# Kernel optimization log

Measured on AMD Instinct MI355X. Metric: run time of the kernel, lower is better.

## Reference

```python
import jax, jax.numpy as jnp
import numpy as np

B, L, H = 64, 1024, 512  # batch, seq_len, hidden_units; encoder feature = 2H


def setup_inputs() -> dict:
    key = jax.random.key(0)
    k1, k2, k3, k4, k5 = jax.random.split(key, 5)
    scale = 1.0 / np.sqrt(3 * H)
    return {
        "hidden": jax.random.normal(k1, (B, H), dtype=jnp.float32),
        "encoder_outputs": jax.random.normal(k2, (B, L, 2 * H), dtype=jnp.float32),
        "W_attn": jax.random.normal(k3, (3 * H, H), dtype=jnp.float32) * scale,
        "b_attn": jax.random.normal(k4, (H,), dtype=jnp.float32) * scale,
        "W_v": jax.random.normal(k5, (H, 1), dtype=jnp.float32) * (1.0 / np.sqrt(H)),
    }


def reference(hidden, encoder_outputs, W_attn, b_attn, W_v):
    # hidden: [B, H] broadcast along seq -> [B, L, H] (torch repeat+transpose)
    b, l, e = encoder_outputs.shape
    h_rep = jnp.broadcast_to(hidden[:, None, :], (b, l, hidden.shape[-1]))
    cat = jnp.concatenate([h_rep, encoder_outputs], axis=-1)     # [B, L, 3H]
    energy = jax.nn.relu(cat @ W_attn + b_attn)                  # [B, L, H]
    attention = (energy @ W_v)[..., 0]                           # [B, L]
    weights = jax.nn.softmax(attention, axis=1)                  # [B, L]
    # bmm([B,1,L], [B,L,E]) -> [B,1,E]
    context = jnp.einsum("bl,ble->be", weights, encoder_outputs)[:, None, :]
    return context
```

## Files before the change

### kernel.cpp

```cpp
#include <hip/hip_runtime.h>
#include <hip/hip_bf16.h>

typedef __attribute__((ext_vector_type(8))) __bf16 bf16x8;
typedef __attribute__((ext_vector_type(4))) float f32x4;


__global__ void qk(const float* __restrict__ hidden, const float* __restrict__ W_attn,
                   const float* __restrict__ b_attn, float* __restrict__ q) {
    int idx = blockIdx.x * 256 + threadIdx.x;
    int b = idx >> 9;
    int h = idx & 511;
    const float* hv = hidden + b * 512;
    float acc = b_attn[h];
#pragma unroll 8
    for (int k = 0; k < 512; ++k)
        acc = fmaf(hv[k], W_attn[(size_t)k * 512 + h], acc);
    q[idx] = acc;
}

__global__ void btk(const float* __restrict__ W_attn, __bf16* __restrict__ Bt) {
    int idx = blockIdx.x * 256 + threadIdx.x;
    int n = idx >> 10;
    int k = idx & 1023;
    Bt[idx] = (__bf16)W_attn[(size_t)(512 + k) * 512 + n];
}

__global__ __launch_bounds__(256, 2) void gemm_logits(
    const float* __restrict__ A, const __bf16* __restrict__ Bt,
    const float* __restrict__ q, const float* __restrict__ Wv,
    float* __restrict__ part)
{
    __shared__ __bf16 As[128][64];
    __shared__ __bf16 Bs[128][64];
    __shared__ float red[128][2];

    const int bid = blockIdx.x;
    const int swz = (bid & 7) * 256 + (bid >> 3);
    const int mt = swz >> 2;
    const int nt = swz & 3;

    const int t = threadIdx.x;
    const int lane = t & 63;
    const int wid = t >> 6;
    const int wm = wid >> 1;
    const int wn = wid & 1;

    const int ar = t >> 3;
    const int ac = (t & 7) * 8;
    const float* Ag = A + (size_t)(mt * 128 + ar) * 1024 + ac;
    const __bf16* Bg = Bt + (size_t)(nt * 128 + ar) * 1024 + ac;

    f32x4 acc[4][4];
#pragma unroll
    for (int m = 0; m < 4; ++m)
#pragma unroll
        for (int n = 0; n < 4; ++n) acc[m][n] = (f32x4)0.0f;

    float4 a0[4], a1[4];
    bf16x8 bv[4];

#define LOADS(K0)                                                              \
    {                                                                          \
        _Pragma("unroll") for (int i = 0; i < 4; ++i) {                        \
            const float* p = Ag + (size_t)i * 32768 + (K0);                    \
            a0[i] = *(const float4*)p;                                         \
            a1[i] = *(const float4*)(p + 4);                                   \
            bv[i] = *(const bf16x8*)(Bg + (size_t)i * 32768 + (K0));           \
        }                                                                      \
    }

    LOADS(0)

    for (int k0 = 0; k0 < 1024; k0 += 64) {
        __syncthreads();
#pragma unroll
        for (int i = 0; i < 4; ++i) {
            bf16x8 v;
            v[0] = (__bf16)a0[i].x; v[1] = (__bf16)a0[i].y;
            v[2] = (__bf16)a0[i].z; v[3] = (__bf16)a0[i].w;
            v[4] = (__bf16)a1[i].x; v[5] = (__bf16)a1[i].y;
            v[6] = (__bf16)a1[i].z; v[7] = (__bf16)a1[i].w;
            *(bf16x8*)&As[ar + i * 32][ac] = v;
            *(bf16x8*)&Bs[ar + i * 32][ac] = bv[i];
        }
        __syncthreads();

        int kn = k0 + 64;
        if (kn < 1024) LOADS(kn)

        const int rsel = (lane & 15);
        const int kb = (lane >> 4) * 8;
#pragma unroll
        for (int ks = 0; ks < 2; ++ks) {
            bf16x8 af[4], bg[4];
#pragma unroll
            for (int m = 0; m < 4; ++m)
                af[m] = *(const bf16x8*)&As[wm * 64 + m * 16 + rsel][ks * 32 + kb];
#pragma unroll
            for (int n = 0; n < 4; ++n)
                bg[n] = *(const bf16x8*)&Bs[wn * 64 + n * 16 + rsel][ks * 32 + kb];
#pragma unroll
            for (int m = 0; m < 4; ++m)
#pragma unroll
                for (int n = 0; n < 4; ++n)
                    acc[m][n] = __builtin_amdgcn_mfma_f32_16x16x32_bf16(
                        af[m], bg[n], acc[m][n], 0, 0, 0);
        }
    }
#undef LOADS

    const int b = mt >> 3;
    const float* qb = q + b * 512;
    float qv[4], wvv[4];
#pragma unroll
    for (int n = 0; n < 4; ++n) {
        int gc = nt * 128 + wn * 64 + n * 16 + (lane & 15);
        qv[n] = qb[gc];
        wvv[n] = Wv[gc];
    }

#pragma unroll
    for (int m = 0; m < 4; ++m) {
#pragma unroll
        for (int j = 0; j < 4; ++j) {
            float s = 0.f;
#pragma unroll
            for (int n = 0; n < 4; ++n) {
                float e = acc[m][n][j] + qv[n];
                s += (e > 0.f ? e : 0.f) * wvv[n];
            }
            s += __shfl_xor(s, 1);
            s += __shfl_xor(s, 2);
            s += __shfl_xor(s, 4);
            s += __shfl_xor(s, 8);
            if ((lane & 15) == 0) {
                int r = wm * 64 + m * 16 + (lane >> 4) * 4 + j;
                red[r][wn] = s;
            }
        }
    }
    __syncthreads();
    if (t < 128) {
        float v = red[t][0] + red[t][1];
        part[(size_t)nt * 65536 + (size_t)mt * 128 + t] = v;
    }
}

__global__ void softmax_k(const float* __restrict__ part, float* __restrict__ w) {
    __shared__ float smx[4];
    __shared__ float ssum[4];
    int b = blockIdx.x;
    int t = threadIdx.x;
    int lane = t & 63, wid = t >> 6;
    float v[4];
    float mx = -3.0e38f;
#pragma unroll
    for (int i = 0; i < 4; ++i) {
        int l = t + i * 256;
        int o = b * 1024 + l;
        float s = part[o] + part[65536 + o] + part[131072 + o] + part[196608 + o];
        v[i] = s;
        mx = fmaxf(mx, s);
    }
#pragma unroll
    for (int off = 32; off >= 1; off >>= 1) mx = fmaxf(mx, __shfl_xor(mx, off));
    if (lane == 0) smx[wid] = mx;
    __syncthreads();
    mx = fmaxf(fmaxf(smx[0], smx[1]), fmaxf(smx[2], smx[3]));
    float e[4];
    float sum = 0.f;
#pragma unroll
    for (int i = 0; i < 4; ++i) { e[i] = __expf(v[i] - mx); sum += e[i]; }
#pragma unroll
    for (int off = 32; off >= 1; off >>= 1) sum += __shfl_xor(sum, off);
    if (lane == 0) ssum[wid] = sum;
    __syncthreads();
    float inv = 1.f / (ssum[0] + ssum[1] + ssum[2] + ssum[3]);
#pragma unroll
    for (int i = 0; i < 4; ++i) w[b * 1024 + t + i * 256] = e[i] * inv;
}

__global__ void ctx_partial(const float* __restrict__ enc, const float* __restrict__ w,
                            float* __restrict__ ctxp) {
    int blk = blockIdx.x;
    int b = blk >> 3;
    int lc = blk & 7;
    int t = threadIdx.x;
    __shared__ float wl[128];
    if (t < 128) wl[t] = w[b * 1024 + lc * 128 + t];
    __syncthreads();
    float4 acc = {0.f, 0.f, 0.f, 0.f};
    const float* base = enc + ((size_t)(b * 1024 + lc * 128)) * 1024 + t * 4;
    for (int l = 0; l < 128; ++l) {
        float4 v = *(const float4*)(base + (size_t)l * 1024);
        float s = wl[l];
        acc.x += s * v.x; acc.y += s * v.y; acc.z += s * v.z; acc.w += s * v.w;
    }
    *(float4*)(ctxp + (size_t)(lc * 64 + b) * 1024 + t * 4) = acc;
}

__global__ void ctx_sum(const float* __restrict__ ctxp, float* __restrict__ out) {
    int idx = blockIdx.x * 256 + threadIdx.x;
    float4 a = {0.f, 0.f, 0.f, 0.f};
#pragma unroll
    for (int lc = 0; lc < 8; ++lc) {
        float4 v = *(const float4*)(ctxp + (size_t)lc * 65536 + (size_t)idx * 4);
        a.x += v.x; a.y += v.y; a.z += v.z; a.w += v.w;
    }
    *(float4*)(out + (size_t)idx * 4) = a;
}

extern "C" void kernel_launch(void* const* d_in, const int* in_sizes, int n_in,
                              void* d_out, int out_size, void* d_ws, size_t ws_size,
                              hipStream_t stream) {
    const float* hidden = (const float*)d_in[0];
    const float* enc    = (const float*)d_in[1];
    const float* W_attn = (const float*)d_in[2];
    const float* b_attn = (const float*)d_in[3];
    const float* W_v    = (const float*)d_in[4];
    float* out = (float*)d_out;

    char* ws = (char*)d_ws;
    float*  q    = (float*)(ws + 0);
    __bf16* Bt   = (__bf16*)(ws + 131072);
    float*  part = (float*)(ws + 1179648);
    float*  wts  = (float*)(ws + 2228224);
    float*  ctxp = (float*)(ws + 2490368);

    qk<<<128, 256, 0, stream>>>(hidden, W_attn, b_attn, q);
    btk<<<2048, 256, 0, stream>>>(W_attn, Bt);
    gemm_logits<<<2048, 256, 0, stream>>>(enc, Bt, q, W_v, part);
    softmax_k<<<64, 256, 0, stream>>>(part, wts);
    ctx_partial<<<512, 256, 0, stream>>>(enc, wts, ctxp);
    ctx_sum<<<64, 256, 0, stream>>>(ctxp, out);
}
```

Before: 192.5 us.

## Compute full N per block with LDS-direct B loads and double buffering

The logits GEMM now gives each 512-thread block the full 512-wide N dimension for a 128-row M tile. Before, four N tiles each re-read and re-converted the same fp32 encoder rows, so those redundant reads are gone, along with the partial-logit buffer and its summation in softmax. The weight matrix is pre-laid out as padded K-tiles (KPAD 40) and streamed into LDS with global_load_lds, double-buffered across 32 K-steps of 32, with one barrier per step. The cost is a much larger LDS footprint and accumulator register set, and only 512 blocks, which may limit occupancy and latency hiding.

```diff
diff --git a/kernel.cpp b/kernel.cpp
--- a/kernel.cpp
+++ b/kernel.cpp
@@ -4,6 +4,9 @@
 typedef __attribute__((ext_vector_type(8))) __bf16 bf16x8;
 typedef __attribute__((ext_vector_type(4))) float f32x4;
 
+
+#define KPAD 40
+#define NKT 32
 
 __global__ void qk(const float* __restrict__ hidden, const float* __restrict__ W_attn,
                    const float* __restrict__ b_attn, float* __restrict__ q) {
@@ -18,103 +21,113 @@
     q[idx] = acc;
 }
 
-__global__ void btk(const float* __restrict__ W_attn, __bf16* __restrict__ Bt) {
+__global__ void btk_img(const float* __restrict__ W_attn, __bf16* __restrict__ Bimg) {
     int idx = blockIdx.x * 256 + threadIdx.x;
-    int n = idx >> 10;
-    int k = idx & 1023;
-    Bt[idx] = (__bf16)W_attn[(size_t)(512 + k) * 512 + n];
-}
-
-__global__ __launch_bounds__(256, 2) void gemm_logits(
-    const float* __restrict__ A, const __bf16* __restrict__ Bt,
-    const float* __restrict__ q, const float* __restrict__ Wv,
-    float* __restrict__ part)
+    int kt = idx / (512 * KPAD);
+    int r  = idx % (512 * KPAD);
+    int n  = r / KPAD;
+    int kk = r % KPAD;
+    float v = (kk < 32) ? W_attn[(size_t)(512 + kt * 32 + kk) * 512 + n] : 0.f;
+    Bimg[idx] = (__bf16)v;
+}
+
+__device__ inline void gl_lds16(const void* g, void* l) {
+    __builtin_amdgcn_global_load_lds(
+        (const __attribute__((address_space(1))) void*)g,
+        (__attribute__((address_space(3))) void*)l, 16, 0, 0);
+}
+
+__global__ __launch_bounds__(512, 2) void gemm_logits2(
+    const float* __restrict__ A,
+    const __bf16* __restrict__ Bimg,
+    const float* __restrict__ q,
+    const float* __restrict__ Wv,
+    float* __restrict__ logits)
 {
-    __shared__ __bf16 As[128][64];
-    __shared__ __bf16 Bs[128][64];
-    __shared__ float red[128][2];
+    __shared__ __bf16 As[2][128 * KPAD];
+    __shared__ __bf16 Bs[2][512 * KPAD];
+    __shared__ float red[128][4];
 
     const int bid = blockIdx.x;
-    const int swz = (bid & 7) * 256 + (bid >> 3);
-    const int mt = swz >> 2;
-    const int nt = swz & 3;
-
+    const int mt = (bid & 7) * 64 + (bid >> 3);
     const int t = threadIdx.x;
     const int lane = t & 63;
     const int wid = t >> 6;
-    const int wm = wid >> 1;
-    const int wn = wid & 1;
-
-    const int ar = t >> 3;
-    const int ac = (t & 7) * 8;
-    const float* Ag = A + (size_t)(mt * 128 + ar) * 1024 + ac;
-    const __bf16* Bg = Bt + (size_t)(nt * 128 + ar) * 1024 + ac;
-
-    f32x4 acc[4][4];
+    const int wm = wid >> 2;
+    const int wn = wid & 3;
+
+    const int ar = t >> 2;
+    const int ak = (t & 3) * 8;
+    const float* Ag = A + (size_t)(mt * 128 + ar) * 1024 + ak;
+    __bf16* AwrBase0 = &As[0][ar * KPAD + ak];
+    __bf16* AwrBase1 = &As[1][ar * KPAD + ak];
+
+    const __bf16* Bg = Bimg + (size_t)(wid * 5) * 512 + lane * 8;
+
+    f32x4 acc[4][8];
 #pragma unroll
     for (int m = 0; m < 4; ++m)
 #pragma unroll
-        for (int n = 0; n < 4; ++n) acc[m][n] = (f32x4)0.0f;
-
-    float4 a0[4], a1[4];
-    bf16x8 bv[4];
-
-#define LOADS(K0)                                                              \
+        for (int n = 0; n < 8; ++n) acc[m][n] = (f32x4)0.0f;
+
+    const int rsel = lane & 15;
+    const int kb = (lane >> 4) * 8;
+
+#define STAGE_B(KT, BUF)                                                       \
     {                                                                          \
-        _Pragma("unroll") for (int i = 0; i < 4; ++i) {                        \
-            const float* p = Ag + (size_t)i * 32768 + (K0);                    \
-            a0[i] = *(const float4*)p;                                         \
-            a1[i] = *(const float4*)(p + 4);                                   \
-            bv[i] = *(const bf16x8*)(Bg + (size_t)i * 32768 + (K0));           \
-        }                                                                      \
-    }
-
-    LOADS(0)
-
-    for (int k0 = 0; k0 < 1024; k0 += 64) {
-        __syncthreads();
-#pragma unroll
-        for (int i = 0; i < 4; ++i) {
+        const __bf16* src = Bg + (size_t)(KT) * (512 * KPAD);                  \
+        _Pragma("unroll") for (int i = 0; i < 5; ++i)                          \
+            gl_lds16(src + i * 512, &Bs[BUF][(wid * 5 + i) * 512]);            \
+    }
+
+    STAGE_B(0, 0)
+    float4 p0 = *(const float4*)Ag;
+    float4 p1 = *(const float4*)(Ag + 4);
+    {
+        bf16x8 v;
+        v[0] = (__bf16)p0.x; v[1] = (__bf16)p0.y; v[2] = (__bf16)p0.z; v[3] = (__bf16)p0.w;
+        v[4] = (__bf16)p1.x; v[5] = (__bf16)p1.y; v[6] = (__bf16)p1.z; v[7] = (__bf16)p1.w;
+        *(bf16x8*)AwrBase0 = v;
+    }
+    __syncthreads();
+
+    for (int kt = 0; kt < NKT; ++kt) {
+        const int cur = kt & 1;
+        if (kt + 1 < NKT) {
+            STAGE_B(kt + 1, cur ^ 1)
+            const float* p = Ag + (kt + 1) * 32;
+            p0 = *(const float4*)p;
+            p1 = *(const float4*)(p + 4);
+        }
+
+        bf16x8 af[4];
+#pragma unroll
+        for (int m = 0; m < 4; ++m)
+            af[m] = *(const bf16x8*)&As[cur][(wm * 64 + m * 16 + rsel) * KPAD + kb];
+#pragma unroll
+        for (int n = 0; n < 8; ++n) {
+            bf16x8 bg = *(const bf16x8*)&Bs[cur][(wn * 128 + n * 16 + rsel) * KPAD + kb];
+#pragma unroll
+            for (int m = 0; m < 4; ++m)
+                acc[m][n] = __builtin_amdgcn_mfma_f32_16x16x32_bf16(
+                    af[m], bg, acc[m][n], 0, 0, 0);
+        }
+
+        if (kt + 1 < NKT) {
             bf16x8 v;
-            v[0] = (__bf16)a0[i].x; v[1] = (__bf16)a0[i].y;
-            v[2] = (__bf16)a0[i].z; v[3] = (__bf16)a0[i].w;
-            v[4] = (__bf16)a1[i].x; v[5] = (__bf16)a1[i].y;
-            v[6] = (__bf16)a1[i].z; v[7] = (__bf16)a1[i].w;
-            *(bf16x8*)&As[ar + i * 32][ac] = v;
-            *(bf16x8*)&Bs[ar + i * 32][ac] = bv[i];
-        }
-        __syncthreads();
-
-        int kn = k0 + 64;
-        if (kn < 1024) LOADS(kn)
-
-        const int rsel = (lane & 15);
-        const int kb = (lane >> 4) * 8;
-#pragma unroll
-        for (int ks = 0; ks < 2; ++ks) {
-            bf16x8 af[4], bg[4];
-#pragma unroll
-            for (int m = 0; m < 4; ++m)
-                af[m] = *(const bf16x8*)&As[wm * 64 + m * 16 + rsel][ks * 32 + kb];
-#pragma unroll
-            for (int n = 0; n < 4; ++n)
-                bg[n] = *(const bf16x8*)&Bs[wn * 64 + n * 16 + rsel][ks * 32 + kb];
-#pragma unroll
-            for (int m = 0; m < 4; ++m)
-#pragma unroll
-                for (int n = 0; n < 4; ++n)
-                    acc[m][n] = __builtin_amdgcn_mfma_f32_16x16x32_bf16(
-                        af[m], bg[n], acc[m][n], 0, 0, 0);
-        }
-    }
-#undef LOADS
-
-    const int b = mt >> 3;
-    const float* qb = q + b * 512;
-    float qv[4], wvv[4];
-#pragma unroll
-    for (int n = 0; n < 4; ++n) {
-        int gc = nt * 128 + wn * 64 + n * 16 + (lane & 15);
+            v[0] = (__bf16)p0.x; v[1] = (__bf16)p0.y; v[2] = (__bf16)p0.z; v[3] = (__bf16)p0.w;
+            v[4] = (__bf16)p1.x; v[5] = (__bf16)p1.y; v[6] = (__bf16)p1.z; v[7] = (__bf16)p1.w;
+            *(bf16x8*)((cur ^ 1) ? AwrBase1 : AwrBase0) = v;
+            __syncthreads();
+        }
+    }
+#undef STAGE_B
+
+    const float* qb = q + (mt >> 3) * 512;
+    float qv[8], wvv[8];
+#pragma unroll
+    for (int n = 0; n < 8; ++n) {
+        int gc = wn * 128 + n * 16 + rsel;
         qv[n] = qb[gc];
         wvv[n] = Wv[gc];
     }
@@ -125,7 +138,7 @@
         for (int j = 0; j < 4; ++j) {
             float s = 0.f;
 #pragma unroll
-            for (int n = 0; n < 4; ++n) {
+            for (int n = 0; n < 8; ++n) {
                 float e = acc[m][n][j] + qv[n];
                 s += (e > 0.f ? e : 0.f) * wvv[n];
             }
@@ -133,20 +146,18 @@
             s += __shfl_xor(s, 2);
             s += __shfl_xor(s, 4);
             s += __shfl_xor(s, 8);
-            if ((lane & 15) == 0) {
+            if (rsel == 0) {
                 int r = wm * 64 + m * 16 + (lane >> 4) * 4 + j;
                 red[r][wn] = s;
             }
         }
     }
     __syncthreads();
-    if (t < 128) {
-        float v = red[t][0] + red[t][1];
-        part[(size_t)nt * 65536 + (size_t)mt * 128 + t] = v;
-    }
-}
-
-__global__ void softmax_k(const float* __restrict__ part, float* __restrict__ w) {
+    if (t < 128)
+        logits[(size_t)mt * 128 + t] = red[t][0] + red[t][1] + red[t][2] + red[t][3];
+}
+
+__global__ void softmax_k(const float* __restrict__ logits, float* __restrict__ w) {
     __shared__ float smx[4];
     __shared__ float ssum[4];
     int b = blockIdx.x;
@@ -156,9 +167,7 @@
     float mx = -3.0e38f;
 #pragma unroll
     for (int i = 0; i < 4; ++i) {
-        int l = t + i * 256;
-        int o = b * 1024 + l;
-        float s = part[o] + part[65536 + o] + part[131072 + o] + part[196608 + o];
+        float s = logits[b * 1024 + t + i * 256];
         v[i] = s;
         mx = fmaxf(mx, s);
     }
@@ -221,16 +230,16 @@
     float* out = (float*)d_out;
 
     char* ws = (char*)d_ws;
-    float*  q    = (float*)(ws + 0);
-    __bf16* Bt   = (__bf16*)(ws + 131072);
-    float*  part = (float*)(ws + 1179648);
-    float*  wts  = (float*)(ws + 2228224);
-    float*  ctxp = (float*)(ws + 2490368);
+    float*  q      = (float*)(ws + 0);
+    __bf16* Bimg   = (__bf16*)(ws + 131072);
+    float*  logits = (float*)(ws + 1441792);
+    float*  wts    = (float*)(ws + 1703936);
+    float*  ctxp   = (float*)(ws + 1966080);
 
     qk<<<128, 256, 0, stream>>>(hidden, W_attn, b_attn, q);
-    btk<<<2048, 256, 0, stream>>>(W_attn, Bt);
-    gemm_logits<<<2048, 256, 0, stream>>>(enc, Bt, q, W_v, part);
-    softmax_k<<<64, 256, 0, stream>>>(part, wts);
+    btk_img<<<2560, 256, 0, stream>>>(W_attn, Bimg);
+    gemm_logits2<<<512, 512, 0, stream>>>(enc, Bimg, q, W_v, logits);
+    softmax_k<<<64, 256, 0, stream>>>(logits, wts);
     ctx_partial<<<512, 256, 0, stream>>>(enc, wts, ctxp);
     ctx_sum<<<64, 256, 0, stream>>>(ctxp, out);
 }
```

Result: slower. 201.8 us (+4.8%).

## Double-buffer GEMM LDS tiles with padded rows and smaller K step

Applied to the files above, without the earlier changes.

Reworks the logits GEMM to use two LDS buffers with a K tile of 32 and padded row stride (40), so each iteration needs only one barrier and the next tile's global loads overlap the MFMA work. Padding is meant to reduce LDS bank conflicts on the fragment reads. Launch bounds are raised to 4 blocks per CU and the reduction scratch reuses the B buffer. The cost is more loop iterations and barriers per K, plus register pressure under the tighter occupancy target.

```diff
diff --git a/kernel.cpp b/kernel.cpp
--- a/kernel.cpp
+++ b/kernel.cpp
@@ -2,8 +2,12 @@
 #include <hip/hip_bf16.h>
 
 typedef __attribute__((ext_vector_type(8))) __bf16 bf16x8;
+typedef __attribute__((ext_vector_type(4))) __bf16 bf16x4;
 typedef __attribute__((ext_vector_type(4))) float f32x4;
 
+
+#define KPAD 40
+#define NKT 32
 
 __global__ void qk(const float* __restrict__ hidden, const float* __restrict__ W_attn,
                    const float* __restrict__ b_attn, float* __restrict__ q) {
@@ -25,14 +29,14 @@
     Bt[idx] = (__bf16)W_attn[(size_t)(512 + k) * 512 + n];
 }
 
-__global__ __launch_bounds__(256, 2) void gemm_logits(
+__global__ __launch_bounds__(256, 4) void gemm_logits3(
     const float* __restrict__ A, const __bf16* __restrict__ Bt,
     const float* __restrict__ q, const float* __restrict__ Wv,
     float* __restrict__ part)
 {
-    __shared__ __bf16 As[128][64];
-    __shared__ __bf16 Bs[128][64];
-    __shared__ float red[128][2];
+    __shared__ __bf16 As[2][128 * KPAD];
+    __shared__ __bf16 Bs[2][128 * KPAD];
+    float* red = (float*)&Bs[0][0];
 
     const int bid = blockIdx.x;
     const int swz = (bid & 7) * 256 + (bid >> 3);
@@ -46,9 +50,11 @@
     const int wn = wid & 1;
 
     const int ar = t >> 3;
-    const int ac = (t & 7) * 8;
+    const int ac = (t & 7) * 4;
     const float* Ag = A + (size_t)(mt * 128 + ar) * 1024 + ac;
-    const __bf16* Bg = Bt + (size_t)(nt * 128 + ar) * 1024 + ac;
+    const int br = t >> 2;
+    const int bc = (t & 3) * 8;
+    const __bf16* Bg = Bt + (size_t)(nt * 128 + br) * 1024 + bc;
 
     f32x4 acc[4][4];
 #pragma unroll
@@ -56,65 +62,69 @@
 #pragma unroll
         for (int n = 0; n < 4; ++n) acc[m][n] = (f32x4)0.0f;
 
-    float4 a0[4], a1[4];
-    bf16x8 bv[4];
+    float4 av[4];
+    bf16x8 bv[2];
 
 #define LOADS(K0)                                                              \
     {                                                                          \
+        _Pragma("unroll") for (int i = 0; i < 4; ++i)                          \
+            av[i] = *(const float4*)(Ag + (size_t)i * 32768 + (K0));           \
+        _Pragma("unroll") for (int i = 0; i < 2; ++i)                          \
+            bv[i] = *(const bf16x8*)(Bg + (size_t)i * 65536 + (K0));           \
+    }
+
+#define WRITES(BUF)                                                            \
+    {                                                                          \
         _Pragma("unroll") for (int i = 0; i < 4; ++i) {                        \
-            const float* p = Ag + (size_t)i * 32768 + (K0);                    \
-            a0[i] = *(const float4*)p;                                         \
-            a1[i] = *(const float4*)(p + 4);                                   \
-            bv[i] = *(const bf16x8*)(Bg + (size_t)i * 32768 + (K0));           \
+            bf16x4 w;                                                          \
+            w[0] = (__bf16)av[i].x; w[1] = (__bf16)av[i].y;                    \
+            w[2] = (__bf16)av[i].z; w[3] = (__bf16)av[i].w;                    \
+            *(bf16x4*)&As[BUF][(ar + i * 32) * KPAD + ac] = w;                 \
         }                                                                      \
+        _Pragma("unroll") for (int i = 0; i < 2; ++i)                          \
+            *(bf16x8*)&Bs[BUF][(br + i * 64) * KPAD + bc] = bv[i];             \
     }
 
     LOADS(0)
-
-    for (int k0 = 0; k0 < 1024; k0 += 64) {
-        __syncthreads();
-#pragma unroll
-        for (int i = 0; i < 4; ++i) {
-            bf16x8 v;
-            v[0] = (__bf16)a0[i].x; v[1] = (__bf16)a0[i].y;
-            v[2] = (__bf16)a0[i].z; v[3] = (__bf16)a0[i].w;
-            v[4] = (__bf16)a1[i].x; v[5] = (__bf16)a1[i].y;
-            v[6] = (__bf16)a1[i].z; v[7] = (__bf16)a1[i].w;
-            *(bf16x8*)&As[ar + i * 32][ac] = v;
-            *(bf16x8*)&Bs[ar + i * 32][ac] = bv[i];
+    WRITES(0)
+    __syncthreads();
+
+    const int rsel = lane & 15;
+    const int kb = (lane >> 4) * 8;
+
+    for (int kt = 0; kt < NKT; ++kt) {
+        const int cur = kt & 1;
+        if (kt + 1 < NKT) LOADS((kt + 1) * 32)
+
+        bf16x8 af[4], bg[4];
+#pragma unroll
+        for (int m = 0; m < 4; ++m)
+            af[m] = *(const bf16x8*)&As[cur][(wm * 64 + m * 16 + rsel) * KPAD + kb];
+#pragma unroll
+        for (int n = 0; n < 4; ++n)
+            bg[n] = *(const bf16x8*)&Bs[cur][(wn * 64 + n * 16 + rsel) * KPAD + kb];
+#pragma unroll
+        for (int m = 0; m < 4; ++m)
+#pragma unroll
+            for (int n = 0; n < 4; ++n)
+                acc[m][n] = __builtin_amdgcn_mfma_f32_16x16x32_bf16(
+                    af[m], bg[n], acc[m][n], 0, 0, 0);
+
+        if (kt + 1 < NKT) {
+            WRITES(cur ^ 1)
+            __syncthreads();
         }
-        __syncthreads();
-
-        int kn = k0 + 64;
-        if (kn < 1024) LOADS(kn)
-
-        const int rsel = (lane & 15);
-        const int kb = (lane >> 4) * 8;
-#pragma unroll
-        for (int ks = 0; ks < 2; ++ks) {
-            bf16x8 af[4], bg[4];
-#pragma unroll
-            for (int m = 0; m < 4; ++m)
-                af[m] = *(const bf16x8*)&As[wm * 64 + m * 16 + rsel][ks * 32 + kb];
-#pragma unroll
-            for (int n = 0; n < 4; ++n)
-                bg[n] = *(const bf16x8*)&Bs[wn * 64 + n * 16 + rsel][ks * 32 + kb];
-#pragma unroll
-            for (int m = 0; m < 4; ++m)
-#pragma unroll
-                for (int n = 0; n < 4; ++n)
-                    acc[m][n] = __builtin_amdgcn_mfma_f32_16x16x32_bf16(
-                        af[m], bg[n], acc[m][n], 0, 0, 0);
-        }
     }
 #undef LOADS
-
-    const int b = mt >> 3;
-    const float* qb = q + b * 512;
+#undef WRITES
+
+    __syncthreads();
+
+    const float* qb = q + (mt >> 3) * 512;
     float qv[4], wvv[4];
 #pragma unroll
     for (int n = 0; n < 4; ++n) {
-        int gc = nt * 128 + wn * 64 + n * 16 + (lane & 15);
+        int gc = nt * 128 + wn * 64 + n * 16 + rsel;
         qv[n] = qb[gc];
         wvv[n] = Wv[gc];
     }
@@ -133,17 +143,15 @@
             s += __shfl_xor(s, 2);
             s += __shfl_xor(s, 4);
             s += __shfl_xor(s, 8);
-            if ((lane & 15) == 0) {
+            if (rsel == 0) {
                 int r = wm * 64 + m * 16 + (lane >> 4) * 4 + j;
-                red[r][wn] = s;
+                red[r * 2 + wn] = s;
             }
         }
     }
     __syncthreads();
-    if (t < 128) {
-        float v = red[t][0] + red[t][1];
-        part[(size_t)nt * 65536 + (size_t)mt * 128 + t] = v;
-    }
+    if (t < 128)
+        part[(size_t)nt * 65536 + (size_t)mt * 128 + t] = red[t * 2] + red[t * 2 + 1];
 }
 
 __global__ void softmax_k(const float* __restrict__ part, float* __restrict__ w) {
@@ -156,8 +164,7 @@
     float mx = -3.0e38f;
 #pragma unroll
     for (int i = 0; i < 4; ++i) {
-        int l = t + i * 256;
-        int o = b * 1024 + l;
+        int o = b * 1024 + t + i * 256;
         float s = part[o] + part[65536 + o] + part[131072 + o] + part[196608 + o];
         v[i] = s;
         mx = fmaxf(mx, s);
@@ -229,7 +236,7 @@
 
     qk<<<128, 256, 0, stream>>>(hidden, W_attn, b_attn, q);
     btk<<<2048, 256, 0, stream>>>(W_attn, Bt);
-    gemm_logits<<<2048, 256, 0, stream>>>(enc, Bt, q, W_v, part);
+    gemm_logits3<<<2048, 256, 0, stream>>>(enc, Bt, q, W_v, part);
     softmax_k<<<64, 256, 0, stream>>>(part, wts);
     ctx_partial<<<512, 256, 0, stream>>>(enc, wts, ctxp);
     ctx_sum<<<64, 256, 0, stream>>>(ctxp, out);
```

Measured after the change: 188.2 us. 2.2% less time.
